# Performance work log

Measured on AMD Instinct MI355X. Metric: run time of the kernel, lower is better.

The kernel has to match this reference:

```python
import jax, jax.numpy as jnp
import numpy as np

B, CIN, COUT, HID, K, H, W = 16, 512, 512, 512, 3, 64, 64

def setup_inputs() -> dict:
    key = jax.random.key(0)
    ks = jax.random.split(key, 8)
    x = jax.random.normal(ks[0], (B, CIN, H, W), dtype=jnp.float32)
    y = jax.random.normal(ks[1], (B, HID), dtype=jnp.float32)
    noise = jax.random.normal(ks[2], (B, 1, H, W), dtype=jnp.float32)
    # params (lrmul=1): weight ~ N(0,1)/sqrt(lrmul), bias zeros
    weight = jax.random.normal(ks[3], (COUT, CIN, K, K), dtype=jnp.float32)
    bias = jnp.zeros((1, COUT, 1, 1), dtype=jnp.float32)
    # ScaleLinear (equalized-lr linear): raw weight ~ N(0,1), runtime scale 1/sqrt(fan_in)
    mod_w = jax.random.normal(ks[4], (CIN, HID), dtype=jnp.float32)
    mod_b = jnp.zeros((CIN,), dtype=jnp.float32)
    noise_scale = jnp.zeros((1,), dtype=jnp.float32)
    return {"x": x, "y": y, "noise": noise, "weight": weight, "bias": bias,
            "mod_w": mod_w, "mod_b": mod_b, "noise_scale": noise_scale}

def reference(x, y, noise, weight, bias, mod_w, mod_b, noise_scale):
    O, I, k, _ = weight.shape
    runtime_coef = 1.0 / np.sqrt(I * k * k)  # gain=1, lrmul=1
    w = weight * runtime_coef                # shared scaled weight [O,I,k,k]
    # style modulation: s = mod(y) + 1, equalized-lr linear scale 1/sqrt(hidden)
    mod_scale = 1.0 / np.sqrt(mod_w.shape[1])
    s = y @ (mod_w.T * mod_scale) + mod_b + 1.0   # [B, I]
    # demodulation coeff without materializing per-sample weights:
    # d[b,o] = rsqrt(sum_{i,kx,ky} (w[o,i]*s[b,i])^2 + eps)
    w2 = jnp.sum(w * w, axis=(2, 3))              # [O, I]
    d = jax.lax.rsqrt(jnp.einsum('oi,bi->bo', w2, s * s) + 1e-8)  # [B, O]
    # fold modulation into input scale, demod into output scale (StyleGAN2 trick;
    # mathematically identical to grouped conv with per-sample weights)
    xm = x * s[:, :, None, None]
    out = jax.lax.conv_general_dilated(
        xm, w, window_strides=(1, 1), padding=((1, 1), (1, 1)),
        dimension_numbers=('NCHW', 'OIHW', 'NCHW'))
    out = out * d[:, :, None, None]
    out = out + noise * noise_scale   # noisy=True, explicit noise input
    out = out + bias                  # lrmul=1
    return out
```

## Files before the change

kernel.cpp:

```cpp
#include <hip/hip_runtime.h>
#include <hip/hip_bf16.h>

typedef unsigned short ushortT;
typedef __attribute__((ext_vector_type(8))) short short8;
typedef __attribute__((ext_vector_type(4))) float f32x4;

#define CIN 512
#define COUTC 512
#define HIDC 512
#define BATCH 16
#define HDIM 64
#define WDIM 64
#define HP 66


__device__ __forceinline__ unsigned short f2bf(float f) {
    __hip_bfloat16 h = __float2bfloat16(f);
    return __builtin_bit_cast(unsigned short, h);
}

__device__ __forceinline__ void gload16(const ushortT* g, ushortT* l) {
    __builtin_amdgcn_global_load_lds(
        (const __attribute__((address_space(1))) void*)g,
        (__attribute__((address_space(3))) void*)l, 16, 0, 0);
}

__global__ void k_style(const float* __restrict__ y, const float* __restrict__ mw,
                        const float* __restrict__ mb, float* __restrict__ s) {
    int lane = threadIdx.x & 63;
    int wid = blockIdx.x * 4 + (threadIdx.x >> 6);
    int b = wid >> 9, i = wid & 511;
    int h0 = lane * 8;
    float4 ya = *(const float4*)(y + b * HIDC + h0);
    float4 yb = *(const float4*)(y + b * HIDC + h0 + 4);
    float4 wa = *(const float4*)(mw + (size_t)i * HIDC + h0);
    float4 wb = *(const float4*)(mw + (size_t)i * HIDC + h0 + 4);
    float v = ya.x*wa.x + ya.y*wa.y + ya.z*wa.z + ya.w*wa.w
            + yb.x*wb.x + yb.y*wb.y + yb.z*wb.z + yb.w*wb.w;
    #pragma unroll
    for (int off = 32; off > 0; off >>= 1) v += __shfl_down(v, off);
    if (lane == 0) s[wid] = v * 0.04419417382415922f + mb[i] + 1.0f;
}

__global__ void k_prepw(const float* __restrict__ w, float* __restrict__ w2,
                        ushortT* __restrict__ wbt) {
    int t = blockIdx.x * 256 + threadIdx.x;
    const float* wp = w + (size_t)t * 9;
    const float coef = 0.014731391274719739f;
    float sum = 0.f;
    #pragma unroll
    for (int k = 0; k < 9; ++k) {
        float v = wp[k] * coef;
        sum += v * v;
        wbt[(size_t)k * (COUTC * CIN) + t] = f2bf(v);
    }
    w2[t] = sum;
}

__global__ void k_demod(const float* __restrict__ w2, const float* __restrict__ s,
                        float* __restrict__ d) {
    int lane = threadIdx.x & 63;
    int wid = blockIdx.x * 4 + (threadIdx.x >> 6);
    int b = wid >> 9, o = wid & 511;
    int i0 = lane * 8;
    float4 wa = *(const float4*)(w2 + (size_t)o * CIN + i0);
    float4 wb = *(const float4*)(w2 + (size_t)o * CIN + i0 + 4);
    float4 sa = *(const float4*)(s + b * CIN + i0);
    float4 sb = *(const float4*)(s + b * CIN + i0 + 4);
    float v = wa.x*sa.x*sa.x + wa.y*sa.y*sa.y + wa.z*sa.z*sa.z + wa.w*sa.w*sa.w
            + wb.x*sb.x*sb.x + wb.y*sb.y*sb.y + wb.z*sb.z*sb.z + wb.w*sb.w*sb.w;
    #pragma unroll
    for (int off = 32; off > 0; off >>= 1) v += __shfl_down(v, off);
    if (lane == 0) d[wid] = rsqrtf(v + 1e-8f);
}

__global__ void k_pad(const float* __restrict__ x, const float* __restrict__ s,
                      ushortT* __restrict__ xpad) {
    __shared__ float tilef[64 * 33];
    int bid = blockIdx.x;
    int cchunk = bid & 15;
    int rem = bid >> 4;
    int prow = rem % HP;
    int b = rem / HP;
    int tid = threadIdx.x;
    size_t rowbase = (((size_t)b * HP + prow) * HP) * CIN + cchunk * 32;
    if (prow == 0 || prow == HP - 1) {
        short8 z = {};
        for (int q = tid; q < HP * 4; q += 256) {
            int col = q >> 2, sub = q & 3;
            *(short8*)(xpad + rowbase + (size_t)col * CIN + sub * 8) = z;
        }
        return;
    }
    int xr = prow - 1;
    int u = tid & 15;
    #pragma unroll
    for (int cl = 0; cl < 32; cl += 16) {
        int c = cl + (tid >> 4);
        float4 v = *(const float4*)(x + (((size_t)b * CIN + cchunk * 32 + c) * HDIM + xr) * WDIM + u * 4);
        float sv = s[b * CIN + cchunk * 32 + c];
        tilef[(u * 4 + 0) * 33 + c] = v.x * sv;
        tilef[(u * 4 + 1) * 33 + c] = v.y * sv;
        tilef[(u * 4 + 2) * 33 + c] = v.z * sv;
        tilef[(u * 4 + 3) * 33 + c] = v.w * sv;
    }
    __syncthreads();
    int col = 1 + (tid >> 2), sub = tid & 3;
    const float* tr = tilef + (col - 1) * 33 + sub * 8;
    short8 o;
    #pragma unroll
    for (int r = 0; r < 8; ++r) o[r] = (short)f2bf(tr[r]);
    *(short8*)(xpad + rowbase + (size_t)col * CIN + sub * 8) = o;
    if (tid < 8) {
        short8 z = {};
        int bcol = (tid < 4) ? 0 : (HP - 1);
        *(short8*)(xpad + rowbase + (size_t)bcol * CIN + (tid & 3) * 8) = z;
    }
}

__global__ __launch_bounds__(256, 2) void k_conv(
    const ushortT* __restrict__ wbt, const ushortT* __restrict__ xpad,
    const float* __restrict__ dcoef, const float* __restrict__ bias,
    const float* __restrict__ noise, const float* __restrict__ nscp,
    float* __restrict__ out)
{
    __shared__ __align__(16) ushortT As[128 * 64];
    __shared__ __align__(16) ushortT Bs[128 * 64];

    int tid = threadIdx.x;
    int lane = tid & 63;
    int wave = tid >> 6;
    int wave_m = wave >> 1, wave_n = wave & 1;

    int bid = blockIdx.x;
    int mtile = bid >> 9;
    int ntile = bid & 511;
    int b = ntile >> 5;
    int h0 = (ntile & 31) << 1;
    int cout0 = mtile << 7;

    size_t asrc[4], bsrc[4];
    #pragma unroll
    for (int call = 0; call < 4; ++call) {
        int a = call * 256 + wave * 64 + lane;
        int row = a >> 3;
        int sub = (a & 7) ^ (row & 7);
        asrc[call] = (size_t)(cout0 + row) * CIN + sub * 8;
        int pr = h0 + (row >> 6);
        int pc = row & 63;
        bsrc[call] = ((size_t)(b * HP + pr) * HP + pc) * CIN + sub * 8;
    }
    ushortT* AsD[4]; ushortT* BsD[4];
    #pragma unroll
    for (int call = 0; call < 4; ++call) {
        AsD[call] = As + call * 2048 + wave * 512;
        BsD[call] = Bs + call * 2048 + wave * 512;
    }

    int l7 = lane & 7;
    int quad = lane >> 4;
    int arow = wave_m * 64 + (lane & 15);
    int brow = wave_n * 64 + (lane & 15);

    f32x4 acc[4][4] = {};

    for (int t = 0; t < 9; ++t) {
        const ushortT* At = wbt + (size_t)t * (COUTC * CIN);
        const ushortT* Bt = xpad + ((size_t)(t / 3) * HP + (t % 3)) * CIN;
        for (int cc = 0; cc < 8; ++cc) {
            int co = cc * 64;
            #pragma unroll
            for (int call = 0; call < 4; ++call) {
                gload16(At + asrc[call] + co, AsD[call]);
                gload16(Bt + bsrc[call] + co, BsD[call]);
            }
            __builtin_amdgcn_s_waitcnt(0);
            __syncthreads();
            #pragma unroll
            for (int kk = 0; kk < 2; ++kk) {
                int slot = ((kk * 4 + quad) ^ l7) * 8;
                short8 af[4], bf[4];
                #pragma unroll
                for (int mi = 0; mi < 4; ++mi)
                    af[mi] = *(const short8*)(As + (arow + mi * 16) * 64 + ((( kk*4+quad) ^ ((arow + mi*16) & 7)) * 8));
                #pragma unroll
                for (int nj = 0; nj < 4; ++nj)
                    bf[nj] = *(const short8*)(Bs + (brow + nj * 16) * 64 + (((kk*4+quad) ^ ((brow + nj*16) & 7)) * 8));
                (void)slot;
                #pragma unroll
                for (int mi = 0; mi < 4; ++mi) {
                    #pragma unroll
                    for (int nj = 0; nj < 4; ++nj)
                        acc[mi][nj] = __builtin_amdgcn_mfma_f32_16x16x32_bf16(
                            af[mi], bf[nj], acc[mi][nj], 0, 0, 0);
                }
            }
            __syncthreads();
        }
    }

    float ns = nscp[0];
    int col = lane & 15, rq = lane >> 4;
    #pragma unroll
    for (int nj = 0; nj < 4; ++nj) {
        int pos = wave_n * 64 + nj * 16 + col;
        int hh = h0 + (pos >> 6), ww = pos & 63;
        float nz = noise[((size_t)b << 12) + (hh << 6) + ww] * ns;
        #pragma unroll
        for (int mi = 0; mi < 4; ++mi) {
            int coutb = cout0 + wave_m * 64 + mi * 16 + rq * 4;
            f32x4 dv = *(const f32x4*)(dcoef + b * COUTC + coutb);
            f32x4 bv = *(const f32x4*)(bias + coutb);
            f32x4 a = acc[mi][nj];
            #pragma unroll
            for (int r = 0; r < 4; ++r) {
                out[(((size_t)(b * COUTC + coutb + r)) << 12) + (hh << 6) + ww]
                    = a[r] * dv[r] + nz + bv[r];
            }
        }
    }
}

extern "C" void kernel_launch(void* const* d_in, const int* in_sizes, int n_in,
                              void* d_out, int out_size, void* d_ws, size_t ws_size,
                              hipStream_t stream) {
    const float* x      = (const float*)d_in[0];
    const float* y      = (const float*)d_in[1];
    const float* noise  = (const float*)d_in[2];
    const float* weight = (const float*)d_in[3];
    const float* bias   = (const float*)d_in[4];
    const float* mod_w  = (const float*)d_in[5];
    const float* mod_b  = (const float*)d_in[6];
    const float* nsc    = (const float*)d_in[7];
    float* out = (float*)d_out;

    char* ws = (char*)d_ws;
    float*   s     = (float*)(ws);
    float*   dcoef = (float*)(ws + 32768);
    float*   w2    = (float*)(ws + 65536);
    ushortT* wbt   = (ushortT*)(ws + 1114112);
    ushortT* xpad  = (ushortT*)(ws + 5832704);

    k_style<<<dim3(2048), dim3(256), 0, stream>>>(y, mod_w, mod_b, s);
    k_prepw<<<dim3(1024), dim3(256), 0, stream>>>(weight, w2, wbt);
    k_demod<<<dim3(2048), dim3(256), 0, stream>>>(w2, s, dcoef);
    k_pad<<<dim3(BATCH * HP * 16), dim3(256), 0, stream>>>(x, s, xpad);
    k_conv<<<dim3(2048), dim3(256), 0, stream>>>(wbt, xpad, dcoef, bias, noise, nsc, out);
}
```

Baseline: 587.8 us.

## Enlarge conv tiles to 256x256 with double-buffered LDS and interleaved MFMA phases

Rewrites the implicit-GEMM conv kernel to use 512-thread blocks computing 256 cout x 256 pixel tiles. The K loop is flattened into 72 steps and global-to-LDS loads for the next step are double-buffered behind MFMA clusters, with s_setprio around the MFMA groups. Block indices are swizzled across XCDs for locality. The aim is to raise operand reuse and hide memory latency. In exchange it uses 128KB of dynamic LDS and 128 accumulator registers per thread, which risks low occupancy and register pressure, and adds more barriers per step.

```diff
diff --git a/kernel.cpp b/kernel.cpp
--- a/kernel.cpp
+++ b/kernel.cpp
@@ -118,85 +118,127 @@
     }
 }
 
-__global__ __launch_bounds__(256, 2) void k_conv(
+#define MFMA_CLUSTER(MH) do { \
+    __builtin_amdgcn_s_setprio(1); \
+    _Pragma("unroll") for (int m_ = 0; m_ < 4; ++m_) { \
+        _Pragma("unroll") for (int n_ = 0; n_ < 4; ++n_) \
+            acc[(MH)*4 + m_][n_] = __builtin_amdgcn_mfma_f32_16x16x32_bf16( \
+                af[m_], bf[n_], acc[(MH)*4 + m_][n_], 0, 0, 0); } \
+    __builtin_amdgcn_s_setprio(0); \
+} while (0)
+
+#define DS_A(MH, KH) do { \
+    _Pragma("unroll") for (int m_ = 0; m_ < 4; ++m_) { \
+        int row_ = wave_m * 128 + (MH)*64 + m_*16 + l15; \
+        af[m_] = *(const short8*)(Ar + row_*64 + ((((KH)*4 + quad) ^ (row_ & 7)) * 8)); \
+    } } while (0)
+
+#define DS_B(KH) do { \
+    _Pragma("unroll") for (int n_ = 0; n_ < 4; ++n_) { \
+        int row_ = wave_n * 64 + n_*16 + l15; \
+        bf[n_] = *(const short8*)(Br + row_*64 + ((((KH)*4 + quad) ^ (row_ & 7)) * 8)); \
+    } } while (0)
+
+__global__ __launch_bounds__(512, 2) void k_conv(
     const ushortT* __restrict__ wbt, const ushortT* __restrict__ xpad,
     const float* __restrict__ dcoef, const float* __restrict__ bias,
     const float* __restrict__ noise, const float* __restrict__ nscp,
     float* __restrict__ out)
 {
-    __shared__ __align__(16) ushortT As[128 * 64];
-    __shared__ __align__(16) ushortT Bs[128 * 64];
+    extern __shared__ __align__(16) ushortT smem[];
 
     int tid = threadIdx.x;
     int lane = tid & 63;
     int wave = tid >> 6;
-    int wave_m = wave >> 1, wave_n = wave & 1;
+    int wave_m = wave >> 2;
+    int wave_n = wave & 3;
+    int l15 = lane & 15;
+    int quad = lane >> 4;
 
     int bid = blockIdx.x;
-    int mtile = bid >> 9;
-    int ntile = bid & 511;
-    int b = ntile >> 5;
-    int h0 = (ntile & 31) << 1;
-    int cout0 = mtile << 7;
-
-    size_t asrc[4], bsrc[4];
-    #pragma unroll
-    for (int call = 0; call < 4; ++call) {
-        int a = call * 256 + wave * 64 + lane;
+    int wg = (bid & 7) * 64 + (bid >> 3);
+    int mtile = wg >> 8;
+    int ntile = wg & 255;
+    int b = ntile >> 4;
+    int h0 = (ntile & 15) << 2;
+    int cout0 = mtile << 8;
+
+    unsigned aoff[4], boff[4], dstE[4];
+    #pragma unroll
+    for (int ca = 0; ca < 4; ++ca) {
+        int a = ca * 512 + tid;
         int row = a >> 3;
         int sub = (a & 7) ^ (row & 7);
-        asrc[call] = (size_t)(cout0 + row) * CIN + sub * 8;
-        int pr = h0 + (row >> 6);
-        int pc = row & 63;
-        bsrc[call] = ((size_t)(b * HP + pr) * HP + pc) * CIN + sub * 8;
-    }
-    ushortT* AsD[4]; ushortT* BsD[4];
-    #pragma unroll
-    for (int call = 0; call < 4; ++call) {
-        AsD[call] = As + call * 2048 + wave * 512;
-        BsD[call] = Bs + call * 2048 + wave * 512;
-    }
-
-    int l7 = lane & 7;
-    int quad = lane >> 4;
-    int arow = wave_m * 64 + (lane & 15);
-    int brow = wave_n * 64 + (lane & 15);
-
-    f32x4 acc[4][4] = {};
-
-    for (int t = 0; t < 9; ++t) {
-        const ushortT* At = wbt + (size_t)t * (COUTC * CIN);
-        const ushortT* Bt = xpad + ((size_t)(t / 3) * HP + (t % 3)) * CIN;
-        for (int cc = 0; cc < 8; ++cc) {
-            int co = cc * 64;
-            #pragma unroll
-            for (int call = 0; call < 4; ++call) {
-                gload16(At + asrc[call] + co, AsD[call]);
-                gload16(Bt + bsrc[call] + co, BsD[call]);
-            }
-            __builtin_amdgcn_s_waitcnt(0);
-            __syncthreads();
-            #pragma unroll
-            for (int kk = 0; kk < 2; ++kk) {
-                int slot = ((kk * 4 + quad) ^ l7) * 8;
-                short8 af[4], bf[4];
-                #pragma unroll
-                for (int mi = 0; mi < 4; ++mi)
-                    af[mi] = *(const short8*)(As + (arow + mi * 16) * 64 + ((( kk*4+quad) ^ ((arow + mi*16) & 7)) * 8));
-                #pragma unroll
-                for (int nj = 0; nj < 4; ++nj)
-                    bf[nj] = *(const short8*)(Bs + (brow + nj * 16) * 64 + (((kk*4+quad) ^ ((brow + nj*16) & 7)) * 8));
-                (void)slot;
-                #pragma unroll
-                for (int mi = 0; mi < 4; ++mi) {
-                    #pragma unroll
-                    for (int nj = 0; nj < 4; ++nj)
-                        acc[mi][nj] = __builtin_amdgcn_mfma_f32_16x16x32_bf16(
-                            af[mi], bf[nj], acc[mi][nj], 0, 0, 0);
-                }
-            }
-            __syncthreads();
-        }
+        aoff[ca] = (unsigned)((cout0 + row) * CIN + sub * 8);
+        int prow = row >> 6;
+        int pcol = row & 63;
+        boff[ca] = (unsigned)((((b * HP) + h0 + prow) * HP + pcol) * CIN + sub * 8);
+        dstE[ca] = (unsigned)(ca * 4096 + wave * 512);
+    }
+
+    f32x4 acc[8][4] = {};
+
+    {
+        const ushortT* Asrc = wbt;
+        const ushortT* Bsrc = xpad;
+        #pragma unroll
+        for (int ca = 0; ca < 4; ++ca) {
+            gload16(Asrc + aoff[ca], smem + dstE[ca]);
+            gload16(Bsrc + boff[ca], smem + 32768 + dstE[ca]);
+        }
+        asm volatile("s_waitcnt vmcnt(0)");
+        __builtin_amdgcn_s_barrier();
+    }
+
+    #pragma unroll 2
+    for (int ks = 0; ks < 72; ++ks) {
+        int cur = ks & 1;
+        const ushortT* Ar = smem + cur * 16384;
+        const ushortT* Br = smem + 32768 + cur * 16384;
+        ushortT* Aw = smem + (cur ^ 1) * 16384;
+        ushortT* Bw = smem + 32768 + (cur ^ 1) * 16384;
+        int ksn = ks + 1;
+        bool st = ksn < 72;
+        int tn = ksn >> 3, ccn = ksn & 7;
+        const ushortT* Asrc = wbt + tn * (COUTC * CIN) + ccn * 64;
+        const ushortT* Bsrc = xpad + ((tn / 3) * HP + (tn % 3)) * CIN + ccn * 64;
+
+        short8 af[4], bf[4];
+
+        if (st) {
+            gload16(Asrc + aoff[0], Aw + dstE[0]); gload16(Bsrc + boff[0], Bw + dstE[0]);
+            gload16(Asrc + aoff[1], Aw + dstE[1]); gload16(Bsrc + boff[1], Bw + dstE[1]);
+        }
+        DS_B(0);
+        DS_A(0, 0);
+        __builtin_amdgcn_s_barrier();
+        asm volatile("s_waitcnt lgkmcnt(0)");
+        MFMA_CLUSTER(0);
+        __builtin_amdgcn_s_barrier();
+
+        if (st) {
+            gload16(Asrc + aoff[2], Aw + dstE[2]); gload16(Bsrc + boff[2], Bw + dstE[2]);
+            gload16(Asrc + aoff[3], Aw + dstE[3]); gload16(Bsrc + boff[3], Bw + dstE[3]);
+        }
+        DS_A(1, 0);
+        __builtin_amdgcn_s_barrier();
+        asm volatile("s_waitcnt lgkmcnt(0)");
+        MFMA_CLUSTER(1);
+        __builtin_amdgcn_s_barrier();
+
+        DS_B(1);
+        DS_A(0, 1);
+        __builtin_amdgcn_s_barrier();
+        asm volatile("s_waitcnt lgkmcnt(0)");
+        MFMA_CLUSTER(0);
+        __builtin_amdgcn_s_barrier();
+
+        DS_A(1, 1);
+        __builtin_amdgcn_s_barrier();
+        asm volatile("s_waitcnt lgkmcnt(0)");
+        MFMA_CLUSTER(1);
+        if (st) asm volatile("s_waitcnt vmcnt(0)");
+        __builtin_amdgcn_s_barrier();
     }
 
     float ns = nscp[0];
@@ -207,8 +249,8 @@
         int hh = h0 + (pos >> 6), ww = pos & 63;
         float nz = noise[((size_t)b << 12) + (hh << 6) + ww] * ns;
         #pragma unroll
-        for (int mi = 0; mi < 4; ++mi) {
-            int coutb = cout0 + wave_m * 64 + mi * 16 + rq * 4;
+        for (int mi = 0; mi < 8; ++mi) {
+            int coutb = cout0 + wave_m * 128 + mi * 16 + rq * 4;
             f32x4 dv = *(const f32x4*)(dcoef + b * COUTC + coutb);
             f32x4 bv = *(const f32x4*)(bias + coutb);
             f32x4 a = acc[mi][nj];
@@ -241,9 +283,16 @@
     ushortT* wbt   = (ushortT*)(ws + 1114112);
     ushortT* xpad  = (ushortT*)(ws + 5832704);
 
+    static bool attr_done = false;
+    if (!attr_done) {
+        (void)hipFuncSetAttribute(reinterpret_cast<const void*>(k_conv),
+                                  hipFuncAttributeMaxDynamicSharedMemorySize, 131072);
+        attr_done = true;
+    }
+
     k_style<<<dim3(2048), dim3(256), 0, stream>>>(y, mod_w, mod_b, s);
     k_prepw<<<dim3(1024), dim3(256), 0, stream>>>(weight, w2, wbt);
     k_demod<<<dim3(2048), dim3(256), 0, stream>>>(w2, s, dcoef);
     k_pad<<<dim3(BATCH * HP * 16), dim3(256), 0, stream>>>(x, s, xpad);
-    k_conv<<<dim3(2048), dim3(256), 0, stream>>>(wbt, xpad, dcoef, bias, noise, nsc, out);
-}
+    k_conv<<<dim3(512), dim3(512), 131072, stream>>>(wbt, xpad, dcoef, bias, noise, nsc, out);
+}
```

New measurement: 529.6 us. -9.9%, faster.
